# Kernel optimization log

Hardware: AMD Instinct MI355X
Metric: run time of the kernel (lower is better)

## Reference

```python
import jax, jax.numpy as jnp
import numpy as np
from jax import lax

T, I, H, L = 4096, 101, 1000, 4  # seq len, letters_num, hidden, num_layers


def setup_inputs() -> dict:
    key = jax.random.key(0)
    ks = jax.random.split(key, 9)
    s = 0.03  # weight scale ~ 1/sqrt(H)
    return {
        "x": jax.random.normal(ks[0], (T, 1, I), jnp.float32),
        "enc_Wih": jax.random.normal(ks[1], (L, 4 * H, I), jnp.float32) * s,
        "enc_Whh": jax.random.normal(ks[2], (L, 4 * H, H), jnp.float32) * s,
        "enc_bih": jax.random.normal(ks[3], (L, 4 * H), jnp.float32) * s,
        "enc_bhh": jax.random.normal(ks[4], (L, 4 * H), jnp.float32) * s,
        "dec_Wih": jax.random.normal(ks[5], (L, 4 * I, H), jnp.float32) * s,
        "dec_Whh": jax.random.normal(ks[6], (L, 4 * I, I), jnp.float32) * s,
        "dec_bih": jax.random.normal(ks[7], (L, 4 * I), jnp.float32) * s,
        "dec_bhh": jax.random.normal(ks[8], (L, 4 * I), jnp.float32) * s,
        "length": T,
    }


def _lstm_cell(x, h, c, Wih, Whh, bih, bhh):
    # PyTorch LSTMCell gate order: i, f, g, o
    gates = x @ Wih.T + bih + h @ Whh.T + bhh  # [T, 4*Hout]
    i, f, g, o = jnp.split(gates, 4, axis=-1)
    c = jax.nn.sigmoid(f) * c + jax.nn.sigmoid(i) * jnp.tanh(g)
    h = jax.nn.sigmoid(o) * jnp.tanh(c)
    return h, c


def _stack(xt, Wih, Whh, bih, bhh, hout):
    # Hidden is reset per timestep in the original, so timesteps are a batch;
    # only the layer chain is sequential. Every layer consumes the same xt.
    t = xt.shape[0]
    init = (jnp.zeros((t, hout), xt.dtype), jnp.zeros((t, hout), xt.dtype))

    def body(carry, p):
        h, c = carry
        wih, whh, bi, bh = p
        h, c = _lstm_cell(xt, h, c, wih, whh, bi, bh)
        return (h, c), None

    (h, _), _ = lax.scan(body, init, (Wih, Whh, bih, bhh))
    return h


def reference(x, enc_Wih, enc_Whh, enc_bih, enc_bhh,
              dec_Wih, dec_Whh, dec_bih, dec_bhh, length):
    xt = x[:, 0, :]                      # [T, I]
    hdim = enc_Whh.shape[-1]
    odim = dec_Whh.shape[-1]
    enc = jax.nn.relu(_stack(xt, enc_Wih, enc_Whh, enc_bih, enc_bhh, hdim))  # [T, H]
    dec = _stack(enc, dec_Wih, dec_Whh, dec_bih, dec_bhh, odim)              # [T, O]
    out = jax.nn.log_softmax(dec, axis=-1)[:, None, :]                       # [T, 1, O]
    return out
```

## Files before the change

kernel.cpp:

```cpp
#include <hip/hip_runtime.h>
#include <cstdint>
#include <cstddef>
#include <cmath>

typedef __bf16 bf16_t;
typedef __bf16 bf16x8 __attribute__((ext_vector_type(8)));
typedef float floatx4 __attribute__((ext_vector_type(4)));

#define AS1 __attribute__((address_space(1)))
#define AS3 __attribute__((address_space(3)))

__device__ __forceinline__ void gload_lds16(const bf16_t* g, bf16_t* l) {
    __builtin_amdgcn_global_load_lds((AS1 void*)(uintptr_t)(g), (AS3 void*)(l), 16, 0, 0);
}

__device__ __forceinline__ float sigf(float x) { return 1.0f / (1.0f + __expf(-x)); }
__device__ __forceinline__ float tanhfast(float x) { return 1.0f - 2.0f / (__expf(2.0f * x) + 1.0f); }

template<int BM>
__global__ __launch_bounds__(256, 4)
void gemm_lstm(const bf16_t* __restrict__ A, const bf16_t* __restrict__ B,
               const float* __restrict__ bias, float* __restrict__ c, int EP,
               bf16_t* __restrict__ hb, int ldH, int hoff, float* __restrict__ hf,
               int K, int ldA, int ldB, int relu)
{
    constexpr int AI = BM / 32;
    __shared__ bf16_t As[BM * 64];
    __shared__ bf16_t Bs[128 * 64];
    const int tid  = threadIdx.x;
    const int lane = tid & 63;
    const int w    = tid >> 6;
    const int wm   = (w & 1) * (BM / 2);
    const int wn   = (w >> 1) * 64;
    const int m0   = blockIdx.y * BM;
    const int n0   = blockIdx.x * 128;

    floatx4 zero = {0.0f, 0.0f, 0.0f, 0.0f};
    floatx4 acc[AI][4];
#pragma unroll
    for (int i = 0; i < AI; ++i)
#pragma unroll
        for (int j = 0; j < 4; ++j) acc[i][j] = zero;

    const int srow = lane >> 3;
    const int sk   = ((lane & 7) ^ srow) * 8;
    const int fr   = lane & 15;
    const int fx   = fr & 7;

    const bf16_t* Ag = A + (size_t)(m0 + srow) * ldA + sk;
    const bf16_t* Bg = B + (size_t)(n0 + srow) * ldB + sk;

    for (int k0 = 0; k0 < K; k0 += 64) {
        __syncthreads();
#pragma unroll
        for (int j = 0; j < AI; ++j) {
            int r0 = (w * AI + j) * 8;
            gload_lds16(Ag + (size_t)r0 * ldA + k0, As + r0 * 64 + lane * 8);
        }
#pragma unroll
        for (int j = 0; j < 4; ++j) {
            int r0 = (w * 4 + j) * 8;
            gload_lds16(Bg + (size_t)r0 * ldB + k0, Bs + r0 * 64 + lane * 8);
        }
        __syncthreads();
#pragma unroll
        for (int kk = 0; kk < 64; kk += 32) {
            const int pc = ((((kk >> 3) + (lane >> 4)) ^ fx) << 3);
            bf16x8 af[AI], bfr[4];
#pragma unroll
            for (int i = 0; i < AI; ++i)
                af[i] = *(const bf16x8*)(As + (wm + i * 16 + fr) * 64 + pc);
#pragma unroll
            for (int j = 0; j < 4; ++j)
                bfr[j] = *(const bf16x8*)(Bs + (wn + j * 16 + fr) * 64 + pc);
#pragma unroll
            for (int i = 0; i < AI; ++i)
#pragma unroll
                for (int j = 0; j < 4; ++j)
                    acc[i][j] = __builtin_amdgcn_mfma_f32_16x16x32_bf16(af[i], bfr[j], acc[i][j], 0, 0, 0);
        }
    }

    const int crow = (lane >> 4) * 4;
    const int ccol = lane & 15;
    const int e    = ((n0 + wn) >> 2) + ccol;
    float bi[4];
#pragma unroll
    for (int j = 0; j < 4; ++j) bi[j] = bias[n0 + wn + j * 16 + ccol];

#pragma unroll
    for (int i = 0; i < AI; ++i) {
#pragma unroll
        for (int r = 0; r < 4; ++r) {
            int t = m0 + wm + i * 16 + crow + r;
            float iv = acc[i][0][r] + bi[0];
            float fv = acc[i][1][r] + bi[1];
            float gv = acc[i][2][r] + bi[2];
            float ov = acc[i][3][r] + bi[3];
            size_t cix = (size_t)t * EP + e;
            float cv = sigf(fv) * c[cix] + sigf(iv) * tanhfast(gv);
            c[cix] = cv;
            float hv = sigf(ov) * tanhfast(cv);
            if (relu) hv = fmaxf(hv, 0.0f);
            if (hb) hb[(size_t)t * ldH + hoff + e] = (bf16_t)hv;
            else    hf[(size_t)t * EP + e] = hv;
        }
    }
}


__global__ void pack_xz(const float* __restrict__ x, bf16_t* __restrict__ Aenc)
{
    int gid = blockIdx.x * 256 + threadIdx.x;
    int row = gid / 144, grp = gid - row * 144;
    int c0  = grp * 8;
    float v[8];
#pragma unroll
    for (int u = 0; u < 8; ++u) v[u] = 0.0f;
    if (c0 < 101) {
        const float* src = x + (size_t)row * 101;
#pragma unroll
        for (int u = 0; u < 8; ++u) { int cc = c0 + u; if (cc < 101) v[u] = src[cc]; }
    }
    bf16x8 o;
#pragma unroll
    for (int u = 0; u < 8; ++u) o[u] = (bf16_t)v[u];
    *(bf16x8*)(Aenc + (size_t)row * 1152 + c0) = o;
}

__global__ void pack_wenc(const float* __restrict__ Wih, const float* __restrict__ Whh,
                          bf16_t* __restrict__ W)
{
    int gid = blockIdx.x * 256 + threadIdx.x;
    int row = gid / 144, grp = gid - row * 144;
    int l = row >> 12, p = row & 4095;
    int g = (p >> 4) & 3, e = ((p >> 6) << 4) + (p & 15);
    int c0 = grp * 8;
    float v[8];
#pragma unroll
    for (int u = 0; u < 8; ++u) v[u] = 0.0f;
    if (e < 1000) {
        size_t r = (size_t)l * 4000 + g * 1000 + e;
        if (c0 >= 128 && c0 < 1128) {
            const float* src = Whh + r * 1000 + (c0 - 128);
            float4 a = *(const float4*)src;
            float4 b = *(const float4*)(src + 4);
            v[0]=a.x; v[1]=a.y; v[2]=a.z; v[3]=a.w; v[4]=b.x; v[5]=b.y; v[6]=b.z; v[7]=b.w;
        } else if (c0 < 128) {
            const float* src = Wih + r * 101;
#pragma unroll
            for (int u = 0; u < 8; ++u) { int cc = c0 + u; if (cc < 101) v[u] = src[cc]; }
        }
    }
    bf16x8 o;
#pragma unroll
    for (int u = 0; u < 8; ++u) o[u] = (bf16_t)v[u];
    *(bf16x8*)(W + (size_t)row * 1152 + c0) = o;
}

__global__ void pack_wdec(const float* __restrict__ Wih, const float* __restrict__ Whh,
                          bf16_t* __restrict__ W)
{
    int gid = blockIdx.x * 256 + threadIdx.x;
    int row = gid / 144, grp = gid - row * 144;
    int l = row >> 9, p = row & 511;
    int g = (p >> 4) & 3, e = ((p >> 6) << 4) + (p & 15);
    int c0 = grp * 8;
    float v[8];
#pragma unroll
    for (int u = 0; u < 8; ++u) v[u] = 0.0f;
    if (e < 101) {
        size_t r = (size_t)l * 404 + g * 101 + e;
        if (c0 < 1000) {
            const float* src = Wih + r * 1000 + c0;
            float4 a = *(const float4*)src;
            float4 b = *(const float4*)(src + 4);
            v[0]=a.x; v[1]=a.y; v[2]=a.z; v[3]=a.w; v[4]=b.x; v[5]=b.y; v[6]=b.z; v[7]=b.w;
        } else if (c0 >= 1024 && c0 < 1128) {
            const float* src = Whh + r * 101;
#pragma unroll
            for (int u = 0; u < 8; ++u) { int cc = c0 + u; if (cc < 1125) v[u] = src[cc - 1024]; }
        }
    }
    bf16x8 o;
#pragma unroll
    for (int u = 0; u < 8; ++u) o[u] = (bf16_t)v[u];
    *(bf16x8*)(W + (size_t)row * 1152 + c0) = o;
}

__global__ void pack_b(const float* __restrict__ ebih, const float* __restrict__ ebhh,
                       const float* __restrict__ dbih, const float* __restrict__ dbhh,
                       float* __restrict__ bse, float* __restrict__ bsd)
{
    int idx = blockIdx.x * 256 + threadIdx.x;
    if (idx < 16384) {
        int l = idx >> 12, p = idx & 4095;
        int g = (p >> 4) & 3, e = ((p >> 6) << 4) + (p & 15);
        bse[idx] = (e < 1000) ? (ebih[l * 4000 + g * 1000 + e] + ebhh[l * 4000 + g * 1000 + e]) : 0.0f;
    } else {
        int k = idx - 16384;
        int l = k >> 9, p = k & 511;
        int g = (p >> 4) & 3, e = ((p >> 6) << 4) + (p & 15);
        bsd[k] = (e < 101) ? (dbih[l * 404 + g * 101 + e] + dbhh[l * 404 + g * 101 + e]) : 0.0f;
    }
}

__global__ void zero_misc(float* __restrict__ cenc, float* __restrict__ cdec,
                          bf16_t* __restrict__ Adec)
{
    int gid = blockIdx.x * 256 + threadIdx.x;
    float4 z = {0.0f, 0.0f, 0.0f, 0.0f};
    if (gid < 1048576) {
        ((float4*)cenc)[gid] = z;
    } else if (gid < 1179648) {
        ((float4*)cdec)[gid - 1048576] = z;
    } else {
        int k = gid - 1179648;
        int row = k >> 4, off = (k & 15) * 8;
        *(float4*)(Adec + (size_t)row * 1152 + 1024 + off) = z;
    }
}

__global__ void log_softmax_k(const float* __restrict__ h, float* __restrict__ out)
{
    int row = blockIdx.x;
    int l   = threadIdx.x;
    const float* hr = h + (size_t)row * 128;
    float v1 = (l < 101)      ? hr[l]      : -INFINITY;
    float v2 = (l + 64 < 101) ? hr[l + 64] : -INFINITY;
    float m = fmaxf(v1, v2);
#pragma unroll
    for (int off = 32; off > 0; off >>= 1) m = fmaxf(m, __shfl_down(m, off));
    m = __shfl(m, 0);
    float ev = ((l < 101) ? __expf(v1 - m) : 0.0f) + ((l + 64 < 101) ? __expf(v2 - m) : 0.0f);
#pragma unroll
    for (int off = 32; off > 0; off >>= 1) ev += __shfl_down(ev, off);
    float lse = m + __logf(__shfl(ev, 0));
    float* orow = out + (size_t)row * 101;
    if (l < 101)      orow[l]      = v1 - lse;
    if (l + 64 < 101) orow[l + 64] = v2 - lse;
}

extern "C" void kernel_launch(void* const* d_in, const int* in_sizes, int n_in,
                              void* d_out, int out_size, void* d_ws, size_t ws_size,
                              hipStream_t stream)
{
    (void)in_sizes; (void)n_in; (void)out_size; (void)ws_size;
    const float* x    = (const float*)d_in[0];
    const float* eWih = (const float*)d_in[1];
    const float* eWhh = (const float*)d_in[2];
    const float* ebih = (const float*)d_in[3];
    const float* ebhh = (const float*)d_in[4];
    const float* dWih = (const float*)d_in[5];
    const float* dWhh = (const float*)d_in[6];
    const float* dbih = (const float*)d_in[7];
    const float* dbhh = (const float*)d_in[8];

    char* ws = (char*)d_ws;
    bf16_t* Aenc = (bf16_t*)(ws);
    bf16_t* Wenc = (bf16_t*)(ws + 9437184);
    bf16_t* Adec = (bf16_t*)(ws + 47185920);
    bf16_t* Wdec = (bf16_t*)(ws + 56623104);
    float*  bse  = (float*) (ws + 61341696);
    float*  bsd  = (float*) (ws + 61407232);
    float*  cenc = (float*) (ws + 61415424);
    float*  cdec = (float*) (ws + 78192640);
    float*  hdec = (float*) (ws + 80289792);

    zero_misc<<<4864, 256, 0, stream>>>(cenc, cdec, Adec);
    pack_xz  <<<2304, 256, 0, stream>>>(x, Aenc);
    pack_wenc<<<9216, 256, 0, stream>>>(eWih, eWhh, Wenc);
    pack_wdec<<<1152, 256, 0, stream>>>(dWih, dWhh, Wdec);
    pack_b   <<<72,   256, 0, stream>>>(ebih, ebhh, dbih, dbhh, bse, bsd);

    for (int l = 0; l < 4; ++l) {
        gemm_lstm<128><<<dim3(32, 32), 256, 0, stream>>>(
            Aenc, Wenc + (size_t)l * 4096 * 1152, bse + l * 4096,
            cenc, 1024,
            (l < 3) ? Aenc : Adec, 1152, (l < 3) ? 128 : 0, nullptr,
            1152, 1152, 1152, (l == 3) ? 1 : 0);
    }
    for (int l = 0; l < 4; ++l) {
        gemm_lstm<64><<<dim3(4, 64), 256, 0, stream>>>(
            Adec, Wdec + (size_t)l * 512 * 1152, bsd + l * 512,
            cdec, 128,
            (l < 3) ? Adec : nullptr, 1152, 1024, (l == 3) ? hdec : nullptr,
            1152, 1152, 1152, 0);
    }
    log_softmax_k<<<4096, 64, 0, stream>>>(hdec, (float*)d_out);
}
```

Measured before the change: 395.8 us.

## Skip zero hidden state in first layer, fuse pack kernels, retile decoder GEMM

The first encoder and decoder layers now shrink K to cover only the input columns, because the hidden state there is zero, and they skip reading the cell state by treating it as zero. This removes the zero_misc memset of cenc, cdec and the Adec pad. The four packing kernels are merged into one launch, and the decoder GEMM switches from BM=64 to BM=32 tiles to run more blocks. One risk: Adec's padding columns 1101..1151 are no longer zeroed. They are multiplied by zero weights, but uninitialised bf16 values could be NaN.

```diff
diff --git a/kernel.cpp b/kernel.cpp
--- a/kernel.cpp
+++ b/kernel.cpp
@@ -22,7 +22,7 @@
 void gemm_lstm(const bf16_t* __restrict__ A, const bf16_t* __restrict__ B,
                const float* __restrict__ bias, float* __restrict__ c, int EP,
                bf16_t* __restrict__ hb, int ldH, int hoff, float* __restrict__ hf,
-               int K, int ldA, int ldB, int relu)
+               int K, int ldA, int ldB, int relu, int czero)
 {
     constexpr int AI = BM / 32;
     __shared__ bf16_t As[BM * 64];
@@ -98,7 +98,9 @@
             float gv = acc[i][2][r] + bi[2];
             float ov = acc[i][3][r] + bi[3];
             size_t cix = (size_t)t * EP + e;
-            float cv = sigf(fv) * c[cix] + sigf(iv) * tanhfast(gv);
+            float cold = 0.0f;
+            if (!czero) cold = c[cix];
+            float cv = sigf(fv) * cold + sigf(iv) * tanhfast(gv);
             c[cix] = cv;
             float hv = sigf(ov) * tanhfast(cv);
             if (relu) hv = fmaxf(hv, 0.0f);
@@ -108,116 +110,96 @@
     }
 }
 
-
-__global__ void pack_xz(const float* __restrict__ x, bf16_t* __restrict__ Aenc)
-{
-    int gid = blockIdx.x * 256 + threadIdx.x;
-    int row = gid / 144, grp = gid - row * 144;
-    int c0  = grp * 8;
-    float v[8];
-#pragma unroll
-    for (int u = 0; u < 8; ++u) v[u] = 0.0f;
-    if (c0 < 101) {
-        const float* src = x + (size_t)row * 101;
-#pragma unroll
-        for (int u = 0; u < 8; ++u) { int cc = c0 + u; if (cc < 101) v[u] = src[cc]; }
-    }
-    bf16x8 o;
-#pragma unroll
-    for (int u = 0; u < 8; ++u) o[u] = (bf16_t)v[u];
-    *(bf16x8*)(Aenc + (size_t)row * 1152 + c0) = o;
-}
-
-__global__ void pack_wenc(const float* __restrict__ Wih, const float* __restrict__ Whh,
-                          bf16_t* __restrict__ W)
-{
-    int gid = blockIdx.x * 256 + threadIdx.x;
-    int row = gid / 144, grp = gid - row * 144;
-    int l = row >> 12, p = row & 4095;
-    int g = (p >> 4) & 3, e = ((p >> 6) << 4) + (p & 15);
-    int c0 = grp * 8;
-    float v[8];
-#pragma unroll
-    for (int u = 0; u < 8; ++u) v[u] = 0.0f;
-    if (e < 1000) {
-        size_t r = (size_t)l * 4000 + g * 1000 + e;
-        if (c0 >= 128 && c0 < 1128) {
-            const float* src = Whh + r * 1000 + (c0 - 128);
-            float4 a = *(const float4*)src;
-            float4 b = *(const float4*)(src + 4);
-            v[0]=a.x; v[1]=a.y; v[2]=a.z; v[3]=a.w; v[4]=b.x; v[5]=b.y; v[6]=b.z; v[7]=b.w;
-        } else if (c0 < 128) {
-            const float* src = Wih + r * 101;
+__global__ void pack_all(const float* __restrict__ x,
+                         const float* __restrict__ eWih, const float* __restrict__ eWhh,
+                         const float* __restrict__ ebih, const float* __restrict__ ebhh,
+                         const float* __restrict__ dWih, const float* __restrict__ dWhh,
+                         const float* __restrict__ dbih, const float* __restrict__ dbhh,
+                         bf16_t* __restrict__ Aenc, bf16_t* __restrict__ Wenc,
+                         bf16_t* __restrict__ Wdec,
+                         float* __restrict__ bse, float* __restrict__ bsd)
+{
+    const int b = blockIdx.x;
+    if (b < 9216) {
+        int gid = b * 256 + threadIdx.x;
+        int row = gid / 144, grp = gid - row * 144;
+        int l = row >> 12, p = row & 4095;
+        int g = (p >> 4) & 3, e = ((p >> 6) << 4) + (p & 15);
+        int c0 = grp * 8;
+        float v[8];
+#pragma unroll
+        for (int u = 0; u < 8; ++u) v[u] = 0.0f;
+        if (e < 1000) {
+            size_t r = (size_t)l * 4000 + g * 1000 + e;
+            if (c0 >= 128 && c0 < 1128) {
+                const float* src = eWhh + r * 1000 + (c0 - 128);
+                float4 a = *(const float4*)src;
+                float4 bq = *(const float4*)(src + 4);
+                v[0]=a.x; v[1]=a.y; v[2]=a.z; v[3]=a.w; v[4]=bq.x; v[5]=bq.y; v[6]=bq.z; v[7]=bq.w;
+            } else if (c0 < 128) {
+                const float* src = eWih + r * 101;
+#pragma unroll
+                for (int u = 0; u < 8; ++u) { int cc = c0 + u; if (cc < 101) v[u] = src[cc]; }
+            }
+        }
+        bf16x8 o;
+#pragma unroll
+        for (int u = 0; u < 8; ++u) o[u] = (bf16_t)v[u];
+        *(bf16x8*)(Wenc + (size_t)row * 1152 + c0) = o;
+    } else if (b < 11520) {
+        int gid = (b - 9216) * 256 + threadIdx.x;
+        int row = gid / 144, grp = gid - row * 144;
+        int c0  = grp * 8;
+        float v[8];
+#pragma unroll
+        for (int u = 0; u < 8; ++u) v[u] = 0.0f;
+        if (c0 < 101) {
+            const float* src = x + (size_t)row * 101;
 #pragma unroll
             for (int u = 0; u < 8; ++u) { int cc = c0 + u; if (cc < 101) v[u] = src[cc]; }
         }
-    }
-    bf16x8 o;
-#pragma unroll
-    for (int u = 0; u < 8; ++u) o[u] = (bf16_t)v[u];
-    *(bf16x8*)(W + (size_t)row * 1152 + c0) = o;
-}
-
-__global__ void pack_wdec(const float* __restrict__ Wih, const float* __restrict__ Whh,
-                          bf16_t* __restrict__ W)
-{
-    int gid = blockIdx.x * 256 + threadIdx.x;
-    int row = gid / 144, grp = gid - row * 144;
-    int l = row >> 9, p = row & 511;
-    int g = (p >> 4) & 3, e = ((p >> 6) << 4) + (p & 15);
-    int c0 = grp * 8;
-    float v[8];
-#pragma unroll
-    for (int u = 0; u < 8; ++u) v[u] = 0.0f;
-    if (e < 101) {
-        size_t r = (size_t)l * 404 + g * 101 + e;
-        if (c0 < 1000) {
-            const float* src = Wih + r * 1000 + c0;
-            float4 a = *(const float4*)src;
-            float4 b = *(const float4*)(src + 4);
-            v[0]=a.x; v[1]=a.y; v[2]=a.z; v[3]=a.w; v[4]=b.x; v[5]=b.y; v[6]=b.z; v[7]=b.w;
-        } else if (c0 >= 1024 && c0 < 1128) {
-            const float* src = Whh + r * 101;
-#pragma unroll
-            for (int u = 0; u < 8; ++u) { int cc = c0 + u; if (cc < 1125) v[u] = src[cc - 1024]; }
-        }
-    }
-    bf16x8 o;
-#pragma unroll
-    for (int u = 0; u < 8; ++u) o[u] = (bf16_t)v[u];
-    *(bf16x8*)(W + (size_t)row * 1152 + c0) = o;
-}
-
-__global__ void pack_b(const float* __restrict__ ebih, const float* __restrict__ ebhh,
-                       const float* __restrict__ dbih, const float* __restrict__ dbhh,
-                       float* __restrict__ bse, float* __restrict__ bsd)
-{
-    int idx = blockIdx.x * 256 + threadIdx.x;
-    if (idx < 16384) {
-        int l = idx >> 12, p = idx & 4095;
+        bf16x8 o;
+#pragma unroll
+        for (int u = 0; u < 8; ++u) o[u] = (bf16_t)v[u];
+        *(bf16x8*)(Aenc + (size_t)row * 1152 + c0) = o;
+    } else if (b < 12672) {
+        int gid = (b - 11520) * 256 + threadIdx.x;
+        int row = gid / 144, grp = gid - row * 144;
+        int l = row >> 9, p = row & 511;
         int g = (p >> 4) & 3, e = ((p >> 6) << 4) + (p & 15);
-        bse[idx] = (e < 1000) ? (ebih[l * 4000 + g * 1000 + e] + ebhh[l * 4000 + g * 1000 + e]) : 0.0f;
+        int c0 = grp * 8;
+        float v[8];
+#pragma unroll
+        for (int u = 0; u < 8; ++u) v[u] = 0.0f;
+        if (e < 101) {
+            size_t r = (size_t)l * 404 + g * 101 + e;
+            if (c0 < 1000) {
+                const float* src = dWih + r * 1000 + c0;
+                float4 a = *(const float4*)src;
+                float4 bq = *(const float4*)(src + 4);
+                v[0]=a.x; v[1]=a.y; v[2]=a.z; v[3]=a.w; v[4]=bq.x; v[5]=bq.y; v[6]=bq.z; v[7]=bq.w;
+            } else if (c0 >= 1024 && c0 < 1128) {
+                const float* src = dWhh + r * 101;
+#pragma unroll
+                for (int u = 0; u < 8; ++u) { int cc = c0 + u; if (cc < 1125) v[u] = src[cc - 1024]; }
+            }
+        }
+        bf16x8 o;
+#pragma unroll
+        for (int u = 0; u < 8; ++u) o[u] = (bf16_t)v[u];
+        *(bf16x8*)(Wdec + (size_t)row * 1152 + c0) = o;
     } else {
-        int k = idx - 16384;
-        int l = k >> 9, p = k & 511;
-        int g = (p >> 4) & 3, e = ((p >> 6) << 4) + (p & 15);
-        bsd[k] = (e < 101) ? (dbih[l * 404 + g * 101 + e] + dbhh[l * 404 + g * 101 + e]) : 0.0f;
-    }
-}
-
-__global__ void zero_misc(float* __restrict__ cenc, float* __restrict__ cdec,
-                          bf16_t* __restrict__ Adec)
-{
-    int gid = blockIdx.x * 256 + threadIdx.x;
-    float4 z = {0.0f, 0.0f, 0.0f, 0.0f};
-    if (gid < 1048576) {
-        ((float4*)cenc)[gid] = z;
-    } else if (gid < 1179648) {
-        ((float4*)cdec)[gid - 1048576] = z;
-    } else {
-        int k = gid - 1179648;
-        int row = k >> 4, off = (k & 15) * 8;
-        *(float4*)(Adec + (size_t)row * 1152 + 1024 + off) = z;
+        int idx = (b - 12672) * 256 + threadIdx.x;
+        if (idx < 16384) {
+            int l = idx >> 12, p = idx & 4095;
+            int g = (p >> 4) & 3, e = ((p >> 6) << 4) + (p & 15);
+            bse[idx] = (e < 1000) ? (ebih[l * 4000 + g * 1000 + e] + ebhh[l * 4000 + g * 1000 + e]) : 0.0f;
+        } else {
+            int k = idx - 16384;
+            int l = k >> 9, p = k & 511;
+            int g = (p >> 4) & 3, e = ((p >> 6) << 4) + (p & 15);
+            bsd[k] = (e < 101) ? (dbih[l * 404 + g * 101 + e] + dbhh[l * 404 + g * 101 + e]) : 0.0f;
+        }
     }
 }
 
@@ -267,25 +249,22 @@
     float*  cdec = (float*) (ws + 78192640);
     float*  hdec = (float*) (ws + 80289792);
 
-    zero_misc<<<4864, 256, 0, stream>>>(cenc, cdec, Adec);
-    pack_xz  <<<2304, 256, 0, stream>>>(x, Aenc);
-    pack_wenc<<<9216, 256, 0, stream>>>(eWih, eWhh, Wenc);
-    pack_wdec<<<1152, 256, 0, stream>>>(dWih, dWhh, Wdec);
-    pack_b   <<<72,   256, 0, stream>>>(ebih, ebhh, dbih, dbhh, bse, bsd);
+    pack_all<<<12744, 256, 0, stream>>>(x, eWih, eWhh, ebih, ebhh, dWih, dWhh, dbih, dbhh,
+                                        Aenc, Wenc, Wdec, bse, bsd);
 
     for (int l = 0; l < 4; ++l) {
         gemm_lstm<128><<<dim3(32, 32), 256, 0, stream>>>(
             Aenc, Wenc + (size_t)l * 4096 * 1152, bse + l * 4096,
             cenc, 1024,
             (l < 3) ? Aenc : Adec, 1152, (l < 3) ? 128 : 0, nullptr,
-            1152, 1152, 1152, (l == 3) ? 1 : 0);
+            (l == 0) ? 128 : 1152, 1152, 1152, (l == 3) ? 1 : 0, (l == 0) ? 1 : 0);
     }
     for (int l = 0; l < 4; ++l) {
-        gemm_lstm<64><<<dim3(4, 64), 256, 0, stream>>>(
+        gemm_lstm<32><<<dim3(4, 128), 256, 0, stream>>>(
             Adec, Wdec + (size_t)l * 512 * 1152, bsd + l * 512,
             cdec, 128,
             (l < 3) ? Adec : nullptr, 1152, 1024, (l == 3) ? hdec : nullptr,
-            1152, 1152, 1152, 0);
+            (l == 0) ? 1024 : 1152, 1152, 1152, 0, (l == 0) ? 1 : 0);
     }
     log_softmax_k<<<4096, 64, 0, stream>>>(hdec, (float*)d_out);
 }
```

After: 354.0 us. 10.5% less time.
